# Kernel optimization log

Measured on AMD Instinct MI355X. Metric: run time of the kernel, lower is better.

Reference implementation:

```python
import jax, jax.numpy as jnp
import numpy as np

NB_KERNEL = 100
DIM_PER_KERNEL = 5


def setup_inputs() -> dict:
    key = jax.random.key(0)
    k1, k2 = jax.random.split(key)
    B, F = 1024, 1024
    x = jax.random.normal(k1, (B, F), dtype=jnp.float32)
    T = jax.random.normal(k2, (F, NB_KERNEL * DIM_PER_KERNEL), dtype=jnp.float32)
    return {"x": x, "T": T}


def reference(x, T):
    B = x.shape[0]
    # project: [B, F] @ [F, K*D] -> [B, K, D]
    m = (x @ T).reshape(B, NB_KERNEL, DIM_PER_KERNEL)
    # pairwise L1 distance over D between all batch rows: [B, K, B]
    # diffs[i, k, d, j] = m[i, k, d] - m[j, k, d]
    diffs = m[:, :, :, None] - jnp.transpose(m, (1, 2, 0))[None, :, :, :]
    l1 = jnp.sum(jnp.abs(diffs), axis=2)  # [B, K, B]
    # exp-kernel similarity summed across batch (includes self term exp(0)=1)
    feat = jnp.sum(jnp.exp(-l1), axis=2)  # [B, K]
    return jnp.concatenate([x, feat], axis=1)  # [B, F + K]
```

## Files before the change

kernel.cpp:

```cpp
#include <hip/hip_runtime.h>
#include <hip/hip_bf16.h>
#include <math.h>

#define B_SZ   1024
#define F_SZ   1024
#define NKER   100
#define DKER   5
#define CCOLS  (NKER * DKER)
#define OUTW   (F_SZ + NKER)
#define LOG2E_F 1.44269504088896340736f

typedef __attribute__((ext_vector_type(8))) short bf16x8;
typedef __attribute__((ext_vector_type(4))) float f32x4;

__device__ __forceinline__ float exp2_hw(float x) {
    float r;
    asm("v_exp_f32 %0, %1" : "=v"(r) : "v"(x));
    return r;
}
__device__ __forceinline__ unsigned cvt_pk_bf16(float lo, float hi) {
    unsigned r;
    asm("v_cvt_pk_bf16_f32 %0, %1, %2" : "=v"(r) : "v"(lo), "v"(hi));
    return r;
}

__global__ __launch_bounds__(256) void init_kernel(const float* __restrict__ x,
                                                   float* __restrict__ out) {
    const int row = blockIdx.x;
    const int t = threadIdx.x;
    const float4 v = *reinterpret_cast<const float4*>(&x[row * F_SZ + t * 4]);
    *reinterpret_cast<float4*>(&out[row * OUTW + t * 4]) = v;
}

#define GAPAD 40

__global__ __launch_bounds__(512) void gemm_block_kernel(const float* __restrict__ x,
                                                         const float* __restrict__ T,
                                                         float* __restrict__ mt) {
    __shared__ short Al[2][32][GAPAD];
    __shared__ short Bl[2][32][GAPAD];
    __shared__ float red[4][64][4];
    const int tid = threadIdx.x;
    const int l = tid & 63;
    const int w = tid >> 6;
    const int h = tid >> 8;
    const int ht = tid & 255;
    const int c0 = blockIdx.x * 32;
    const int j0 = blockIdx.y * 32;
    const int fh = h * (F_SZ / 2);

    const int sac = ht & 31;
    const int sak = (ht >> 5) * 4;
    const int cldA = (c0 + sac < CCOLS) ? (c0 + sac) : (CCOLS - 1);
    const int sbj = ht >> 3;
    const int sbk = (ht & 7) * 4;

    const int q = w & 3;
    const int cq = (q & 1) * 16;
    const int jq = (q >> 1) * 16;
    const int fr = (l >> 4) * 8;
    const int ar = cq + (l & 15);
    const int br = jq + (l & 15);

    f32x4 acc = {0.f, 0.f, 0.f, 0.f};

    for (int s = 0; s < 16; ++s) {
        const int fb = fh + s * 32;
        const float a0 = T[(fb + sak + 0) * CCOLS + cldA];
        const float a1 = T[(fb + sak + 1) * CCOLS + cldA];
        const float a2 = T[(fb + sak + 2) * CCOLS + cldA];
        const float a3 = T[(fb + sak + 3) * CCOLS + cldA];
        const float4 b = *reinterpret_cast<const float4*>(&x[(j0 + sbj) * F_SZ + fb + sbk]);
        if (s) __syncthreads();
        {
            uint2 aw; aw.x = cvt_pk_bf16(a0, a1); aw.y = cvt_pk_bf16(a2, a3);
            *reinterpret_cast<uint2*>(&Al[h][sac][sak]) = aw;
            uint2 bw; bw.x = cvt_pk_bf16(b.x, b.y); bw.y = cvt_pk_bf16(b.z, b.w);
            *reinterpret_cast<uint2*>(&Bl[h][sbj][sbk]) = bw;
        }
        __syncthreads();
        const bf16x8 af = *reinterpret_cast<const bf16x8*>(&Al[h][ar][fr]);
        const bf16x8 bf = *reinterpret_cast<const bf16x8*>(&Bl[h][br][fr]);
        acc = __builtin_amdgcn_mfma_f32_16x16x32_bf16(af, bf, acc, 0, 0, 0);
    }

    if (h == 1) {
        #pragma unroll
        for (int qq = 0; qq < 4; ++qq) red[q][l][qq] = acc[qq];
    }
    __syncthreads();
    if (h == 0) {
        const int jst = j0 + jq + (l & 15);
        const int cst = c0 + cq + (l >> 4) * 4;
        #pragma unroll
        for (int qq = 0; qq < 4; ++qq) {
            const int c = cst + qq;
            if (c < CCOLS)
                mt[c * B_SZ + jst] = (acc[qq] + red[q][l][qq]) * LOG2E_F;
        }
    }
}

__global__ __launch_bounds__(256) void pair_kernel(const float* __restrict__ mt,
                                                   float* __restrict__ out) {
    __shared__ float mj[DKER][B_SZ];
    __shared__ float red[256];
    const int tid = threadIdx.x;
    const int bx = blockIdx.x;
    const int k = blockIdx.y;
    const int cb = k * DKER;

    #pragma unroll
    for (int d = 0; d < DKER; ++d) {
        const float4 v = *reinterpret_cast<const float4*>(&mt[(cb + d) * B_SZ + tid * 4]);
        *reinterpret_cast<float4*>(&mj[d][tid * 4]) = v;
    }
    __syncthreads();

    const int lane = tid & 63;
    const int w = tid >> 6;
    const int i = bx * 64 + lane;
    const float a0 = mj[0][i], a1 = mj[1][i], a2 = mj[2][i],
                a3 = mj[3][i], a4 = mj[4][i];

    float acc = 0.f;
    const int jbase = w * 256;
    #pragma unroll 4
    for (int jb = 0; jb < 64; ++jb) {
        const int j4 = jbase + jb * 4;
        const float4 q0 = *reinterpret_cast<const float4*>(&mj[0][j4]);
        const float4 q1 = *reinterpret_cast<const float4*>(&mj[1][j4]);
        const float4 q2 = *reinterpret_cast<const float4*>(&mj[2][j4]);
        const float4 q3 = *reinterpret_cast<const float4*>(&mj[3][j4]);
        const float4 q4 = *reinterpret_cast<const float4*>(&mj[4][j4]);
#define DOJ(C) { \
        const float d0 = a0 - q0.C; \
        const float d1 = a1 - q1.C; \
        const float d2 = a2 - q2.C; \
        const float d3 = a3 - q3.C; \
        const float d4 = a4 - q4.C; \
        const float p01 = fabsf(d0) + fabsf(d1); \
        const float p23 = fabsf(d2) + fabsf(d3); \
        const float p234 = p23 + fabsf(d4); \
        acc += exp2_hw(-p01 - p234); }
        DOJ(x) DOJ(y) DOJ(z) DOJ(w)
#undef DOJ
    }

    red[tid] = acc;
    __syncthreads();
    if (tid < 64) {
        const float s = red[tid] + red[tid + 64] + red[tid + 128] + red[tid + 192];
        out[(bx * 64 + tid) * OUTW + F_SZ + k] = s;
    }
}

extern "C" void kernel_launch(void* const* d_in, const int* in_sizes, int n_in,
                              void* d_out, int out_size, void* d_ws, size_t ws_size,
                              hipStream_t stream) {
    const float* x = (const float*)d_in[0];
    const float* T = (const float*)d_in[1];
    float* out = (float*)d_out;
    float* mt = (float*)d_ws;

    init_kernel<<<dim3(B_SZ), 256, 0, stream>>>(x, out);
    gemm_block_kernel<<<dim3(16, 32), 512, 0, stream>>>(x, T, mt);
    pair_kernel<<<dim3(B_SZ / 64, NKER), 256, 0, stream>>>(mt, out);
}
```

Baseline: 111.9 us.

## Pre-stage x as bf16 MFMA fragments and read pair operands via scalar loads

Adds a staging kernel that converts x to bf16 in MFMA fragment order. A new LDS-free GEMM kernel then has one wave per 16x16 tile and reads T directly from global memory, with no barriers. The pair kernel drops its LDS staging and instead streams the j-operands with wave-uniform s_load_dwordx4 into SGPRs, removing LDS reads from the inner loop. The cost is an extra kernel launch, a workspace requirement (with a fallback to the old GEMM), and a full lgkmcnt wait on every iteration that may stall the exp loop.

```diff
diff --git a/kernel.cpp b/kernel.cpp
--- a/kernel.cpp
+++ b/kernel.cpp
@@ -30,6 +30,67 @@
     const int t = threadIdx.x;
     const float4 v = *reinterpret_cast<const float4*>(&x[row * F_SZ + t * 4]);
     *reinterpret_cast<float4*>(&out[row * OUTW + t * 4]) = v;
+}
+
+__global__ __launch_bounds__(256) void stage_xb_kernel(const float* __restrict__ x,
+                                                       short* __restrict__ xb) {
+    const int tid = blockIdx.x * 256 + threadIdx.x;
+    const int l = tid & 63;
+    const int g = tid >> 6;
+    const int jt = g >> 5, s = g & 31;
+    const int j = jt * 16 + (l & 15);
+    const int kb = s * 32 + (l >> 4) * 8;
+    const float4 v0 = *reinterpret_cast<const float4*>(&x[j * F_SZ + kb]);
+    const float4 v1 = *reinterpret_cast<const float4*>(&x[j * F_SZ + kb + 4]);
+    uint4 w;
+    w.x = cvt_pk_bf16(v0.x, v0.y);
+    w.y = cvt_pk_bf16(v0.z, v0.w);
+    w.z = cvt_pk_bf16(v1.x, v1.y);
+    w.w = cvt_pk_bf16(v1.z, v1.w);
+    *reinterpret_cast<uint4*>(&xb[(size_t)g * 512 + l * 8]) = w;
+}
+
+__global__ __launch_bounds__(256) void gemm_frag_kernel(const float* __restrict__ T,
+                                                        const short* __restrict__ xb,
+                                                        float* __restrict__ mt) {
+    const int tid = threadIdx.x;
+    const int l = tid & 63;
+    const int w = tid >> 6;
+    const int tile = blockIdx.x * 4 + w;
+    const int ct = tile & 31, jt = tile >> 5;
+    const int lr = l & 15;
+    const int lk = (l >> 4) * 8;
+    const int cA = ct * 16 + lr;
+    const int cL = (cA < CCOLS) ? cA : (CCOLS - 1);
+
+    const float* ap = T + (size_t)lk * CCOLS + cL;
+    const short* bp = xb + ((size_t)(jt * 32) * 512 + l * 8);
+
+    f32x4 acc = {0.f, 0.f, 0.f, 0.f};
+    #pragma unroll 4
+    for (int s = 0; s < 32; ++s) {
+        const float a0 = ap[0 * CCOLS], a1 = ap[1 * CCOLS];
+        const float a2 = ap[2 * CCOLS], a3 = ap[3 * CCOLS];
+        const float a4 = ap[4 * CCOLS], a5 = ap[5 * CCOLS];
+        const float a6 = ap[6 * CCOLS], a7 = ap[7 * CCOLS];
+        const bf16x8 bf = *reinterpret_cast<const bf16x8*>(bp);
+        ap += 32 * CCOLS;
+        bp += 512;
+        union { unsigned u[4]; bf16x8 v; } A;
+        A.u[0] = cvt_pk_bf16(a0, a1);
+        A.u[1] = cvt_pk_bf16(a2, a3);
+        A.u[2] = cvt_pk_bf16(a4, a5);
+        A.u[3] = cvt_pk_bf16(a6, a7);
+        acc = __builtin_amdgcn_mfma_f32_16x16x32_bf16(A.v, bf, acc, 0, 0, 0);
+    }
+
+    const int jst = jt * 16 + lr;
+    const int cst = ct * 16 + (l >> 4) * 4;
+    #pragma unroll
+    for (int q = 0; q < 4; ++q) {
+        const int c = cst + q;
+        if (c < CCOLS) mt[c * B_SZ + jst] = acc[q] * LOG2E_F;
+    }
 }
 
 #define GAPAD 40
@@ -103,48 +164,48 @@
 
 __global__ __launch_bounds__(256) void pair_kernel(const float* __restrict__ mt,
                                                    float* __restrict__ out) {
-    __shared__ float mj[DKER][B_SZ];
     __shared__ float red[256];
     const int tid = threadIdx.x;
     const int bx = blockIdx.x;
     const int k = blockIdx.y;
     const int cb = k * DKER;
-
-    #pragma unroll
-    for (int d = 0; d < DKER; ++d) {
-        const float4 v = *reinterpret_cast<const float4*>(&mt[(cb + d) * B_SZ + tid * 4]);
-        *reinterpret_cast<float4*>(&mj[d][tid * 4]) = v;
-    }
-    __syncthreads();
-
     const int lane = tid & 63;
-    const int w = tid >> 6;
+    const int wu = __builtin_amdgcn_readfirstlane(tid >> 6);
     const int i = bx * 64 + lane;
-    const float a0 = mj[0][i], a1 = mj[1][i], a2 = mj[2][i],
-                a3 = mj[3][i], a4 = mj[4][i];
+
+    const float a0 = mt[(cb + 0) * B_SZ + i];
+    const float a1 = mt[(cb + 1) * B_SZ + i];
+    const float a2 = mt[(cb + 2) * B_SZ + i];
+    const float a3 = mt[(cb + 3) * B_SZ + i];
+    const float a4 = mt[(cb + 4) * B_SZ + i];
+
+    unsigned long long base =
+        (unsigned long long)(uintptr_t)(mt + (size_t)cb * B_SZ + wu * 256);
 
     float acc = 0.f;
-    const int jbase = w * 256;
-    #pragma unroll 4
     for (int jb = 0; jb < 64; ++jb) {
-        const int j4 = jbase + jb * 4;
-        const float4 q0 = *reinterpret_cast<const float4*>(&mj[0][j4]);
-        const float4 q1 = *reinterpret_cast<const float4*>(&mj[1][j4]);
-        const float4 q2 = *reinterpret_cast<const float4*>(&mj[2][j4]);
-        const float4 q3 = *reinterpret_cast<const float4*>(&mj[3][j4]);
-        const float4 q4 = *reinterpret_cast<const float4*>(&mj[4][j4]);
-#define DOJ(C) { \
-        const float d0 = a0 - q0.C; \
-        const float d1 = a1 - q1.C; \
-        const float d2 = a2 - q2.C; \
-        const float d3 = a3 - q3.C; \
-        const float d4 = a4 - q4.C; \
+        f32x4 q0, q1, q2, q3, q4;
+        asm("s_load_dwordx4 %0, %[p], 0x0\n\t"
+            "s_load_dwordx4 %1, %[p], 0x1000\n\t"
+            "s_load_dwordx4 %2, %[p], 0x2000\n\t"
+            "s_load_dwordx4 %3, %[p], 0x3000\n\t"
+            "s_load_dwordx4 %4, %[p], 0x4000\n\t"
+            "s_waitcnt lgkmcnt(0)"
+            : "=s"(q0), "=s"(q1), "=s"(q2), "=s"(q3), "=s"(q4)
+            : [p] "s"(base));
+#define DOJ(E) { \
+        const float d0 = q0[E] - a0; \
+        const float d1 = q1[E] - a1; \
+        const float d2 = q2[E] - a2; \
+        const float d3 = q3[E] - a3; \
+        const float d4 = q4[E] - a4; \
         const float p01 = fabsf(d0) + fabsf(d1); \
         const float p23 = fabsf(d2) + fabsf(d3); \
         const float p234 = p23 + fabsf(d4); \
         acc += exp2_hw(-p01 - p234); }
-        DOJ(x) DOJ(y) DOJ(z) DOJ(w)
+        DOJ(0) DOJ(1) DOJ(2) DOJ(3)
 #undef DOJ
+        base += 16;
     }
 
     red[tid] = acc;
@@ -162,8 +223,17 @@
     const float* T = (const float*)d_in[1];
     float* out = (float*)d_out;
     float* mt = (float*)d_ws;
+    short* xb = (short*)((char*)d_ws + (size_t)CCOLS * B_SZ * sizeof(float));
+
+    const size_t need = (size_t)CCOLS * B_SZ * sizeof(float)
+                      + (size_t)2048 * 512 * sizeof(short);
 
     init_kernel<<<dim3(B_SZ), 256, 0, stream>>>(x, out);
-    gemm_block_kernel<<<dim3(16, 32), 512, 0, stream>>>(x, T, mt);
+    if (ws_size >= need) {
+        stage_xb_kernel<<<dim3(512), 256, 0, stream>>>(x, xb);
+        gemm_frag_kernel<<<dim3(512), 256, 0, stream>>>(T, xb, mt);
+    } else {
+        gemm_block_kernel<<<dim3(16, 32), 512, 0, stream>>>(x, T, mt);
+    }
     pair_kernel<<<dim3(B_SZ / 64, NKER), 256, 0, stream>>>(mt, out);
 }
```

Result: slower. 115.9 us (+3.7%).
